# Kernel tuning notes

Measured on AMD Instinct MI355X. Metric: run time of the kernel, lower is better.

The kernel has to match this reference:

```python
import jax, jax.numpy as jnp
import numpy as np

B, S, D = 8, 2048, 768
H, HD = 12, 64  # num_heads, head_dim = embed_dim // num_heads
EPS = 1e-6


def setup_inputs() -> dict:
    key = jax.random.key(0)
    ks = jax.random.split(key, 9)
    sc = 0.02
    return {
        "x": jax.random.normal(ks[0], (B, S, D), jnp.float32),
        "Wq": jax.random.normal(ks[1], (H, D, HD), jnp.float32) * sc,
        "bq": jax.random.normal(ks[2], (H, HD), jnp.float32) * sc,
        "Wk": jax.random.normal(ks[3], (H, D, HD), jnp.float32) * sc,
        "bk": jax.random.normal(ks[4], (H, HD), jnp.float32) * sc,
        "Wv": jax.random.normal(ks[5], (H, D, HD), jnp.float32) * sc,
        "bv": jax.random.normal(ks[6], (H, HD), jnp.float32) * sc,
        "Wp": jax.random.normal(ks[7], (D, D), jnp.float32) * sc,
        "bp": jax.random.normal(ks[8], (D,), jnp.float32) * sc,
    }


def reference(x, Wq, bq, Wk, bk, Wv, bv, Wp, bp):
    # Batched per-head projections (the torch loop over heads, vectorized).
    Q = jnp.einsum("bsd,hde->bhse", x, Wq) + bq[:, None, :]  # [B,H,S,HD]
    K = jnp.einsum("bsd,hde->bhse", x, Wk) + bk[:, None, :]
    V = jnp.einsum("bsd,hde->bhse", x, Wv) + bv[:, None, :]
    scale = jnp.sqrt(jnp.float32(HD)) + EPS  # intended 1/sqrt(head_dim) scaling
    scores = jnp.einsum("bhse,bhte->bhst", Q, K) / scale  # [B,H,S,S]
    attn = jax.nn.softmax(scores, axis=-1)
    ctx = jnp.einsum("bhst,bhte->bhse", attn, V)  # [B,H,S,HD]
    # concat heads along last dim (head i -> slice i*HD:(i+1)*HD), then project
    ctx = jnp.transpose(ctx, (0, 2, 1, 3)).reshape(B, S, H * HD)
    return ctx @ Wp + bp
```

## Files before the change

### kernel.cpp

```cpp
#include <hip/hip_runtime.h>
#include <hip/hip_bf16.h>
#include <stdint.h>

#define B_  8
#define S_  2048
#define D_  768
#define H_  12
#define HD_ 64
#define BH_ (B_*H_)
#define M_  (B_*S_)

typedef __bf16 bf16;
typedef __bf16 bf16x8 __attribute__((ext_vector_type(8)));
typedef __bf16 bf16x4 __attribute__((ext_vector_type(4)));
typedef short  short4v __attribute__((ext_vector_type(4)));
typedef float  f32x4  __attribute__((ext_vector_type(4)));

#define QSCALE2 0.18033685756901243f

#if __has_builtin(__builtin_amdgcn_exp2f)
#define EXP2(x) __builtin_amdgcn_exp2f(x)
#else
#define EXP2(x) exp2f(x)
#endif

#define LDS_BARRIER() asm volatile("s_waitcnt lgkmcnt(0)\n\ts_barrier" ::: "memory")

#define GLD16(gptr, lptr) __builtin_amdgcn_global_load_lds( \
    (const __attribute__((address_space(1))) uint32_t*)(gptr), \
    (__attribute__((address_space(3))) uint32_t*)(lptr), 16, 0, 0)

#if __has_builtin(__builtin_amdgcn_mfma_f32_16x16x16bf16_1k)
static __device__ inline f32x4 mfma16(bf16x4 a, bf16x4 b, f32x4 c) {
  return __builtin_amdgcn_mfma_f32_16x16x16bf16_1k(
      __builtin_bit_cast(short4v, a), __builtin_bit_cast(short4v, b), c, 0, 0, 0);
}
#else
static __device__ inline f32x4 mfma16(bf16x4 a, bf16x4 b, f32x4 c) {
  bf16 z = (bf16)0.f;
  bf16x8 a8 = {a[0], a[1], a[2], a[3], z, z, z, z};
  bf16x8 b8 = {b[0], b[1], b[2], b[3], z, z, z, z};
  return __builtin_amdgcn_mfma_f32_16x16x32_bf16(a8, b8, c, 0, 0, 0);
}
#endif

__global__ __launch_bounds__(256) void f2b(const float* __restrict__ src,
                                           bf16* __restrict__ dst, int n) {
  int i = (blockIdx.x * 256 + threadIdx.x) * 8;
  if (i >= n) return;
  float4 a = *(const float4*)(src + i);
  float4 b = *(const float4*)(src + i + 4);
  bf16 o[8] = {(bf16)a.x, (bf16)a.y, (bf16)a.z, (bf16)a.w,
               (bf16)b.x, (bf16)b.y, (bf16)b.z, (bf16)b.w};
  *(uint4*)(dst + i) = *(const uint4*)o;
}

__global__ __launch_bounds__(256) void transpose64_f2b(const float* __restrict__ src,
                                                       bf16* __restrict__ dst,
                                                       int R, int C) {
  __shared__ bf16 t[64][72];
  int mat = blockIdx.z;
  const float* s = src + (size_t)mat * R * C;
  bf16* d = dst + (size_t)mat * C * R;
  int r0 = blockIdx.x * 64, c0 = blockIdx.y * 64;
  int tid = threadIdx.x;
  #pragma unroll
  for (int it = 0; it < 4; ++it) {
    int i = (tid >> 4) + it * 16;
    int j = (tid & 15) * 4;
    float4 v = *(const float4*)(s + (size_t)(r0 + i) * C + c0 + j);
    t[j + 0][i] = (bf16)v.x; t[j + 1][i] = (bf16)v.y;
    t[j + 2][i] = (bf16)v.z; t[j + 3][i] = (bf16)v.w;
  }
  __syncthreads();
  #pragma unroll
  for (int it = 0; it < 4; ++it) {
    int i = (tid >> 4) + it * 16;
    int j = (tid & 15) * 4;
    bf16* p = d + (size_t)(c0 + i) * R + r0 + j;
    p[0] = t[i][j]; p[1] = t[i][j + 1]; p[2] = t[i][j + 2]; p[3] = t[i][j + 3];
  }
}

__global__ void pack_bias(const float* __restrict__ bq, const float* __restrict__ bk,
                          const float* __restrict__ bv, float* __restrict__ ball) {
  int i = blockIdx.x * 256 + threadIdx.x;
  if (i < 2304) {
    float v = (i < 768) ? bq[i] : (i < 1536 ? bk[i - 768] : bv[i - 1536]);
    ball[i] = v;
  }
}

template <int MODE>
__global__ __launch_bounds__(256, 2) void gemm_bt(
    const bf16* __restrict__ A, const bf16* __restrict__ Bt,
    const float* __restrict__ bias, float* __restrict__ C,
    bf16* __restrict__ Qo, bf16* __restrict__ Ko, bf16* __restrict__ Vo,
    int Mdim, int Ndim, int Kdim)
{
  __shared__ bf16 As[128 * 32];
  __shared__ bf16 Bs[128 * 32];
  int tid = threadIdx.x;
  int wave = tid >> 6, lane = tid & 63;
  int wm = wave & 1, wn = wave >> 1;
  int m0 = blockIdx.x * 128, n0 = blockIdx.y * 128;
  int lm = lane & 15, lq = lane >> 4;

  int c0_ = wave * 2;
  int r_in = lane >> 2;
  int ps   = lane & 3;
  int rowA0 = c0_ * 16 + r_in;
  int rowA1 = rowA0 + 16;
  int ls0 = ps ^ (rowA0 & 3);
  int ls1 = ps ^ (rowA1 & 3);

  f32x4 zero = {0.f, 0.f, 0.f, 0.f};
  f32x4 acc[4][4];
  #pragma unroll
  for (int i = 0; i < 4; ++i)
    #pragma unroll
    for (int j = 0; j < 4; ++j) acc[i][j] = zero;

  for (int k0 = 0; k0 < Kdim; k0 += 32) {
    __syncthreads();
    {
      const bf16* ga0 = A  + (size_t)(m0 + rowA0) * Kdim + k0 + ls0 * 8;
      const bf16* ga1 = A  + (size_t)(m0 + rowA1) * Kdim + k0 + ls1 * 8;
      const bf16* gb0 = Bt + (size_t)(n0 + rowA0) * Kdim + k0 + ls0 * 8;
      const bf16* gb1 = Bt + (size_t)(n0 + rowA1) * Kdim + k0 + ls1 * 8;
      GLD16(ga0, &As[c0_ * 512]);
      GLD16(ga1, &As[c0_ * 512 + 512]);
      GLD16(gb0, &Bs[c0_ * 512]);
      GLD16(gb1, &Bs[c0_ * 512 + 512]);
    }
    __syncthreads();

    bf16x8 af[4], bfr[4];
    #pragma unroll
    for (int i = 0; i < 4; ++i) {
      int ra = wm * 64 + i * 16 + lm;
      af[i] = *(const bf16x8*)(&As[ra * 32 + ((lq ^ (ra & 3)) * 8)]);
    }
    #pragma unroll
    for (int j = 0; j < 4; ++j) {
      int rb = wn * 64 + j * 16 + lm;
      bfr[j] = *(const bf16x8*)(&Bs[rb * 32 + ((lq ^ (rb & 3)) * 8)]);
    }
    #pragma unroll
    for (int i = 0; i < 4; ++i)
      #pragma unroll
      for (int j = 0; j < 4; ++j)
        acc[i][j] = __builtin_amdgcn_mfma_f32_16x16x32_bf16(af[i], bfr[j], acc[i][j], 0, 0, 0);
  }

  int mbase = m0 + wm * 64, nbase = n0 + wn * 64;
  #pragma unroll
  for (int j = 0; j < 4; ++j) {
    int n = nbase + j * 16 + lm;
    float bv_ = bias[n];
    if (MODE == 0) {
      #pragma unroll
      for (int i = 0; i < 4; ++i)
        #pragma unroll
        for (int r = 0; r < 4; ++r) {
          int m = mbase + i * 16 + lq * 4 + r;
          C[(size_t)m * Ndim + n] = acc[i][j][r] + bv_;
        }
    } else {
      int which = n / 768;
      int rem = n - which * 768;
      int h = rem >> 6, e = rem & 63;
      float scl = (which == 0) ? QSCALE2 : 1.0f;
      if (which == 2) {
        #pragma unroll
        for (int i = 0; i < 4; ++i)
          #pragma unroll
          for (int r = 0; r < 4; ++r) {
            int m = mbase + i * 16 + lq * 4 + r;
            int b = m >> 11, s = m & 2047;
            Vo[((size_t)(b * H_ + h) * 64 + e) * S_ + s] = (bf16)(acc[i][j][r] + bv_);
          }
      } else {
        bf16* dst = (which == 0) ? Qo : Ko;
        #pragma unroll
        for (int i = 0; i < 4; ++i)
          #pragma unroll
          for (int r = 0; r < 4; ++r) {
            int m = mbase + i * 16 + lq * 4 + r;
            int b = m >> 11, s = m & 2047;
            dst[((size_t)(b * H_ + h) * S_ + s) * 64 + e] = (bf16)((acc[i][j][r] + bv_) * scl);
          }
      }
    }
  }
}

__global__ __launch_bounds__(256, 4) void flash_attn(
    const bf16* __restrict__ Q, const bf16* __restrict__ K,
    const bf16* __restrict__ Vt, bf16* __restrict__ ctx)
{
  __shared__ bf16 smem[16384];
  int tid = threadIdx.x;
  int wave = tid >> 6, lane = tid & 63;
  int lm = lane & 15, lq = lane >> 4;
  int x7 = lane & 7;

  int id = blockIdx.x;
  int xcd = id & 7, jj = id >> 3;
  int bh = xcd * 12 + (jj >> 4);
  int q0 = (jj & 15) * 128;

  const bf16* Qb = Q + (size_t)bh * S_ * 64;
  const bf16* Kb = K + (size_t)bh * S_ * 64;
  const bf16* Vb = Vt + (size_t)bh * 64 * S_;

  int rr = lane >> 3;
  int ls = (lane & 7) ^ rr;
  const bf16* gk0 = Kb + (size_t)(wave * 16 + rr) * 64 + ls * 8;
  const bf16* gv0 = Vb + (size_t)(wave * 16 + rr) * S_ + ls * 8;

  {
    const bf16* gq = Qb + (size_t)(q0 + wave * 32 + rr) * 64 + ls * 8;
    #pragma unroll
    for (int c = 0; c < 4; ++c)
      GLD16(gq + (size_t)c * 512, &smem[8192 + (wave * 4 + c) * 512]);
    GLD16(gk0,                    &smem[wave * 1024]);
    GLD16(gk0 + 512,              &smem[wave * 1024 + 512]);
    GLD16(gv0,                    &smem[4096 + wave * 1024]);
    GLD16(gv0 + (size_t)8 * S_,   &smem[4096 + wave * 1024 + 512]);
  }
  __syncthreads();

  int qw = wave * 32;
  bf16x8 qf[2][2];
  #pragma unroll
  for (int ks = 0; ks < 2; ++ks)
    #pragma unroll
    for (int mi = 0; mi < 2; ++mi)
      qf[ks][mi] = *(const bf16x8*)(&smem[8192 + (qw + mi * 16 + lm) * 64
                                          + ((ks * 4 + lq) ^ x7) * 8]);
  LDS_BARRIER();

  f32x4 zero = {0.f, 0.f, 0.f, 0.f};
  f32x4 O[2][4];
  float lsum[2] = {0.f, 0.f};
  #pragma unroll
  for (int i = 0; i < 2; ++i)
    #pragma unroll
    for (int d = 0; d < 4; ++d) O[i][d] = zero;

  for (int t = 0; t < 32; ++t) {
    int cb = (t & 1) << 13;
    int nb = 8192 - cb;

    if (t + 1 < 32) {
      const bf16* gk = gk0 + (size_t)(t + 1) * 4096;
      const bf16* gv = gv0 + (size_t)(t + 1) * 64;
      GLD16(gk,                   &smem[nb + wave * 1024]);
      GLD16(gk + 512,             &smem[nb + wave * 1024 + 512]);
      GLD16(gv,                   &smem[nb + 4096 + wave * 1024]);
      GLD16(gv + (size_t)8 * S_,  &smem[nb + 4096 + wave * 1024 + 512]);
    }

    f32x4 sacc[2][4];
    #pragma unroll
    for (int i = 0; i < 2; ++i)
      #pragma unroll
      for (int j = 0; j < 4; ++j) sacc[i][j] = zero;
    __builtin_amdgcn_s_setprio(1);
    #pragma unroll
    for (int ks = 0; ks < 2; ++ks) {
      #pragma unroll
      for (int ni = 0; ni < 4; ++ni) {
        bf16x8 ak = *(const bf16x8*)(&smem[cb + (ni * 16 + lm) * 64
                                           + ((ks * 4 + lq) ^ x7) * 8]);
        sacc[0][ni] = __builtin_amdgcn_mfma_f32_16x16x32_bf16(ak, qf[ks][0], sacc[0][ni], 0, 0, 0);
        sacc[1][ni] = __builtin_amdgcn_mfma_f32_16x16x32_bf16(ak, qf[ks][1], sacc[1][ni], 0, 0, 0);
      }
    }
    __builtin_amdgcn_s_setprio(0);

    bf16x4 pexp[2][4];
    #pragma unroll
    for (int mi = 0; mi < 2; ++mi) {
      #pragma unroll
      for (int ni = 0; ni < 4; ++ni) {
        float e0 = EXP2(sacc[mi][ni][0]);
        float e1 = EXP2(sacc[mi][ni][1]);
        float e2 = EXP2(sacc[mi][ni][2]);
        float e3 = EXP2(sacc[mi][ni][3]);
        lsum[mi] += (e0 + e1) + (e2 + e3);
        bf16x4 px = {(bf16)e0, (bf16)e1, (bf16)e2, (bf16)e3};
        pexp[mi][ni] = px;
      }
    }

    __builtin_amdgcn_s_setprio(1);
    #pragma unroll
    for (int ni = 0; ni < 4; ++ni) {
      #pragma unroll
      for (int dj = 0; dj < 4; ++dj) {
        bf16x4 vb = *(const bf16x4*)(&smem[cb + 4096 + (dj * 16 + lm) * 64
                                           + ((ni * 2 + (lq >> 1)) ^ x7) * 8
                                           + (lq & 1) * 4]);
        O[0][dj] = mfma16(pexp[0][ni], vb, O[0][dj]);
        O[1][dj] = mfma16(pexp[1][ni], vb, O[1][dj]);
      }
    }
    __builtin_amdgcn_s_setprio(0);

    asm volatile("s_waitcnt vmcnt(0)" ::: "memory");
    LDS_BARRIER();
  }

  float ls_[2];
  #pragma unroll
  for (int mi = 0; mi < 2; ++mi) {
    float rs = lsum[mi];
    rs += __shfl_xor(rs, 16);
    rs += __shfl_xor(rs, 32);
    ls_[mi] = rs;
  }

  int b = bh / H_, h = bh % H_;
  #pragma unroll
  for (int mi = 0; mi < 2; ++mi) {
    #pragma unroll
    for (int r = 0; r < 4; ++r) {
      int s = q0 + qw + mi * 16 + lq * 4 + r;
      float lv = __shfl(ls_[mi], lq * 4 + r);
      float linv = 1.0f / lv;
      #pragma unroll
      for (int dj = 0; dj < 4; ++dj) {
        int d = dj * 16 + lm;
        ctx[(size_t)(b * S_ + s) * D_ + h * 64 + d] = (bf16)(O[mi][dj][r] * linv);
      }
    }
  }
}

extern "C" void kernel_launch(void* const* d_in, const int* in_sizes, int n_in,
                              void* d_out, int out_size, void* d_ws, size_t ws_size,
                              hipStream_t stream)
{
  const float* x  = (const float*)d_in[0];
  const float* Wq = (const float*)d_in[1];
  const float* bq = (const float*)d_in[2];
  const float* Wk = (const float*)d_in[3];
  const float* bk = (const float*)d_in[4];
  const float* Wv = (const float*)d_in[5];
  const float* bv = (const float*)d_in[6];
  const float* Wp = (const float*)d_in[7];
  const float* bp = (const float*)d_in[8];
  float* out = (float*)d_out;

  char* w = (char*)d_ws;
  const size_t SZ  = (size_t)BH_ * S_ * 64;
  const size_t SZb = SZ * sizeof(bf16);
  bf16*  xb   = (bf16*)(w);
  bf16*  Qb   = (bf16*)(w + 1 * SZb);
  bf16*  Kb   = (bf16*)(w + 2 * SZb);
  bf16*  Vtb  = (bf16*)(w + 3 * SZb);
  bf16*  Wt   = (bf16*)(w + 4 * SZb);
  bf16*  Wpt  = Wt;
  float* ball = (float*)(w + 4 * SZb + 2304 * 768 * 2);
  bf16*  ctx  = xb;

  f2b<<<(int)(SZ / (256 * 8)), 256, 0, stream>>>(x, xb, (int)SZ);
  transpose64_f2b<<<dim3(12, 1, 12), 256, 0, stream>>>(Wq, Wt,                      768, 64);
  transpose64_f2b<<<dim3(12, 1, 12), 256, 0, stream>>>(Wk, Wt + (size_t)768 * 768,  768, 64);
  transpose64_f2b<<<dim3(12, 1, 12), 256, 0, stream>>>(Wv, Wt + (size_t)1536 * 768, 768, 64);
  pack_bias<<<9, 256, 0, stream>>>(bq, bk, bv, ball);

  gemm_bt<1><<<dim3(128, 18), 256, 0, stream>>>(xb, Wt, ball, (float*)nullptr,
                                                Qb, Kb, Vtb, M_, 2304, 768);
  transpose64_f2b<<<dim3(12, 12, 1), 256, 0, stream>>>(Wp, Wpt, 768, 768);
  flash_attn<<<1536, 256, 0, stream>>>(Qb, Kb, Vtb, ctx);
  gemm_bt<0><<<dim3(128, 6), 256, 0, stream>>>(ctx, Wpt, bp, out,
                                               (bf16*)nullptr, (bf16*)nullptr, (bf16*)nullptr,
                                               M_, 768, 768);
}
```

Measured before the change: 386.0 us.

## Double-buffer GEMM LDS tiles and fuse weight-prep kernels into one launch

The GEMM main loop now uses two LDS buffers, so the global-to-LDS loads for the next K-step are issued before the MFMAs on the current one. It also raises wave priority around the MFMA block and keeps a single barrier per iteration. Separately, the three QKV weight transposes and the bias pack are merged into one prep kernel to cut launch overhead. LDS per block doubles to 32KB, which may affect occupancy at two blocks per CU.

```diff
diff --git a/kernel.cpp b/kernel.cpp
--- a/kernel.cpp
+++ b/kernel.cpp
@@ -82,12 +82,42 @@
   }
 }
 
-__global__ void pack_bias(const float* __restrict__ bq, const float* __restrict__ bk,
-                          const float* __restrict__ bv, float* __restrict__ ball) {
-  int i = blockIdx.x * 256 + threadIdx.x;
-  if (i < 2304) {
-    float v = (i < 768) ? bq[i] : (i < 1536 ? bk[i - 768] : bv[i - 1536]);
-    ball[i] = v;
+__global__ __launch_bounds__(256) void prep_w(
+    const float* __restrict__ Wq, const float* __restrict__ Wk,
+    const float* __restrict__ Wv, const float* __restrict__ bq,
+    const float* __restrict__ bk, const float* __restrict__ bv,
+    bf16* __restrict__ Wt, float* __restrict__ ball)
+{
+  int z = blockIdx.z;
+  int tid = threadIdx.x;
+  if (z == 36) {
+    int i = blockIdx.x * 256 + tid;
+    if (i < 2304) {
+      float v = (i < 768) ? bq[i] : (i < 1536 ? bk[i - 768] : bv[i - 1536]);
+      ball[i] = v;
+    }
+    return;
+  }
+  __shared__ bf16 t[64][72];
+  int w = z / 12, h = z % 12;
+  const float* s = (w == 0 ? Wq : (w == 1 ? Wk : Wv)) + (size_t)h * 768 * 64;
+  bf16* d = Wt + (size_t)z * 64 * 768;
+  int r0 = blockIdx.x * 64;
+  #pragma unroll
+  for (int it = 0; it < 4; ++it) {
+    int i = (tid >> 4) + it * 16;
+    int j = (tid & 15) * 4;
+    float4 v = *(const float4*)(s + (size_t)(r0 + i) * 64 + j);
+    t[j + 0][i] = (bf16)v.x; t[j + 1][i] = (bf16)v.y;
+    t[j + 2][i] = (bf16)v.z; t[j + 3][i] = (bf16)v.w;
+  }
+  __syncthreads();
+  #pragma unroll
+  for (int it = 0; it < 4; ++it) {
+    int i = (tid >> 4) + it * 16;
+    int j = (tid & 15) * 4;
+    bf16* p = d + (size_t)i * 768 + r0 + j;
+    p[0] = t[i][j]; p[1] = t[i][j + 1]; p[2] = t[i][j + 2]; p[3] = t[i][j + 3];
   }
 }
 
@@ -98,8 +128,7 @@
     bf16* __restrict__ Qo, bf16* __restrict__ Ko, bf16* __restrict__ Vo,
     int Mdim, int Ndim, int Kdim)
 {
-  __shared__ bf16 As[128 * 32];
-  __shared__ bf16 Bs[128 * 32];
+  __shared__ bf16 smem[16384];
   int tid = threadIdx.x;
   int wave = tid >> 6, lane = tid & 63;
   int wm = wave & 1, wn = wave >> 1;
@@ -121,36 +150,47 @@
     #pragma unroll
     for (int j = 0; j < 4; ++j) acc[i][j] = zero;
 
-  for (int k0 = 0; k0 < Kdim; k0 += 32) {
-    __syncthreads();
-    {
-      const bf16* ga0 = A  + (size_t)(m0 + rowA0) * Kdim + k0 + ls0 * 8;
-      const bf16* ga1 = A  + (size_t)(m0 + rowA1) * Kdim + k0 + ls1 * 8;
-      const bf16* gb0 = Bt + (size_t)(n0 + rowA0) * Kdim + k0 + ls0 * 8;
-      const bf16* gb1 = Bt + (size_t)(n0 + rowA1) * Kdim + k0 + ls1 * 8;
-      GLD16(ga0, &As[c0_ * 512]);
-      GLD16(ga1, &As[c0_ * 512 + 512]);
-      GLD16(gb0, &Bs[c0_ * 512]);
-      GLD16(gb1, &Bs[c0_ * 512 + 512]);
-    }
-    __syncthreads();
+  int NK = Kdim >> 5;
+
+  GLD16(A  + (size_t)(m0 + rowA0) * Kdim + ls0 * 8, &smem[c0_ * 512]);
+  GLD16(A  + (size_t)(m0 + rowA1) * Kdim + ls1 * 8, &smem[c0_ * 512 + 512]);
+  GLD16(Bt + (size_t)(n0 + rowA0) * Kdim + ls0 * 8, &smem[4096 + c0_ * 512]);
+  GLD16(Bt + (size_t)(n0 + rowA1) * Kdim + ls1 * 8, &smem[4096 + c0_ * 512 + 512]);
+  __syncthreads();
+
+  for (int kk = 0; kk < NK; ++kk) {
+    int cb = (kk & 1) << 13;
+    int nb = 8192 - cb;
+
+    if (kk + 1 < NK) {
+      int k0 = (kk + 1) * 32;
+      GLD16(A  + (size_t)(m0 + rowA0) * Kdim + k0 + ls0 * 8, &smem[nb + c0_ * 512]);
+      GLD16(A  + (size_t)(m0 + rowA1) * Kdim + k0 + ls1 * 8, &smem[nb + c0_ * 512 + 512]);
+      GLD16(Bt + (size_t)(n0 + rowA0) * Kdim + k0 + ls0 * 8, &smem[nb + 4096 + c0_ * 512]);
+      GLD16(Bt + (size_t)(n0 + rowA1) * Kdim + k0 + ls1 * 8, &smem[nb + 4096 + c0_ * 512 + 512]);
+    }
 
     bf16x8 af[4], bfr[4];
     #pragma unroll
     for (int i = 0; i < 4; ++i) {
       int ra = wm * 64 + i * 16 + lm;
-      af[i] = *(const bf16x8*)(&As[ra * 32 + ((lq ^ (ra & 3)) * 8)]);
+      af[i] = *(const bf16x8*)(&smem[cb + ra * 32 + ((lq ^ (ra & 3)) * 8)]);
     }
     #pragma unroll
     for (int j = 0; j < 4; ++j) {
       int rb = wn * 64 + j * 16 + lm;
-      bfr[j] = *(const bf16x8*)(&Bs[rb * 32 + ((lq ^ (rb & 3)) * 8)]);
-    }
+      bfr[j] = *(const bf16x8*)(&smem[cb + 4096 + rb * 32 + ((lq ^ (rb & 3)) * 8)]);
+    }
+    __builtin_amdgcn_s_setprio(1);
     #pragma unroll
     for (int i = 0; i < 4; ++i)
       #pragma unroll
       for (int j = 0; j < 4; ++j)
         acc[i][j] = __builtin_amdgcn_mfma_f32_16x16x32_bf16(af[i], bfr[j], acc[i][j], 0, 0, 0);
+    __builtin_amdgcn_s_setprio(0);
+
+    asm volatile("s_waitcnt vmcnt(0)" ::: "memory");
+    LDS_BARRIER();
   }
 
   int mbase = m0 + wm * 64, nbase = n0 + wn * 64;
@@ -367,10 +407,7 @@
   bf16*  ctx  = xb;
 
   f2b<<<(int)(SZ / (256 * 8)), 256, 0, stream>>>(x, xb, (int)SZ);
-  transpose64_f2b<<<dim3(12, 1, 12), 256, 0, stream>>>(Wq, Wt,                      768, 64);
-  transpose64_f2b<<<dim3(12, 1, 12), 256, 0, stream>>>(Wk, Wt + (size_t)768 * 768,  768, 64);
-  transpose64_f2b<<<dim3(12, 1, 12), 256, 0, stream>>>(Wv, Wt + (size_t)1536 * 768, 768, 64);
-  pack_bias<<<9, 256, 0, stream>>>(bq, bk, bv, ball);
+  prep_w<<<dim3(12, 1, 37), 256, 0, stream>>>(Wq, Wk, Wv, bq, bk, bv, Wt, ball);
 
   gemm_bt<1><<<dim3(128, 18), 256, 0, stream>>>(xb, Wt, ball, (float*)nullptr,
                                                 Qb, Kb, Vtb, M_, 2304, 768);
```

Result: faster. 369.1 us (-4.4%).
